# Optimization experiments

Measured on AMD Instinct MI355X. Metric: run time of the kernel, lower is better.

## Reference

```python
import jax, jax.numpy as jnp
import numpy as np

B, T, D, H = 2, 2048, 1024, 16
HD = D // H  # head_dim = 64


def setup_inputs() -> dict:
    key = jax.random.key(0)
    k1, k2, k3 = jax.random.split(key, 3)
    s = 0.02
    return {
        "x": jax.random.normal(k1, (B, T, D), dtype=jnp.float32),
        "Wqkv": jax.random.normal(k2, (D, 3 * D), dtype=jnp.float32) * s,
        "bqkv": jnp.zeros((3 * D,), dtype=jnp.float32),
        "Wout": jax.random.normal(k3, (D, D), dtype=jnp.float32) * s,
        "bout": jnp.zeros((D,), dtype=jnp.float32),
    }


def reference(x, Wqkv, bqkv, Wout, bout):
    Bx, Tx, Dx = x.shape
    qkv = x @ Wqkv + bqkv                                  # [B,T,3D]
    qkv = qkv.reshape(Bx, Tx, 3, H, HD)
    q, k, v = (jnp.moveaxis(qkv, 2, 0)[i] for i in range(3))  # each [B,T,H,HD]
    q = q.transpose(0, 2, 1, 3)  # [B,H,T,HD]
    k = k.transpose(0, 2, 1, 3)
    v = v.transpose(0, 2, 1, 3)
    scale = 1.0 / jnp.sqrt(jnp.float32(HD))
    attn = jnp.einsum("bhqd,bhkd->bhqk", q, k) * scale     # [B,H,T,T]
    causal = jnp.tril(jnp.ones((Tx, Tx), dtype=bool))
    attn = jnp.where(causal, attn, -jnp.inf)
    attn = jax.nn.softmax(attn, axis=-1)
    out = jnp.einsum("bhqk,bhkd->bhqd", attn, v)           # [B,H,T,HD]
    out = out.transpose(0, 2, 1, 3).reshape(Bx, Tx, Dx)
    return out @ Wout + bout
```

## Files before the change

### kernel.cpp

```cpp
#include <hip/hip_runtime.h>
#include <hip/hip_bf16.h>
#include <hip/hip_fp16.h>

typedef __attribute__((ext_vector_type(8))) short bf16x8;
typedef __attribute__((ext_vector_type(4))) float f32x4;
typedef unsigned short u16;
typedef unsigned int uint;

#define Bb 2
#define Tt 2048
#define Dd 1024
#define Hh 16

#define EXP2F(x) __builtin_amdgcn_exp2f(x)

__device__ inline u16 f2bf(float f) {
    union { float f; uint u; } v; v.f = f;
    uint r = v.u + 0x7fffu + ((v.u >> 16) & 1u);
    return (u16)(r >> 16);
}
__device__ inline uint fbits(float f) { union { float f; uint u; } v; v.f = f; return v.u; }
__device__ inline u16 f2h(float f) { return __half_as_ushort(__float2half(f)); }
__device__ inline float h2f(u16 u) { return __half2float(__ushort_as_half(u)); }

__device__ inline void glds16(const u16* g, u16* l) {
    __builtin_amdgcn_global_load_lds(
        (const __attribute__((address_space(1))) void*)g,
        (__attribute__((address_space(3))) void*)l,
        16, 0, 0);
}

__global__ __launch_bounds__(256) void cvt_bf16(
    const float* __restrict__ in, u16* __restrict__ out)
{
    const size_t i = ((size_t)blockIdx.x * 256 + threadIdx.x) * 8;
    const float4 a = *(const float4*)&in[i];
    const float4 b = *(const float4*)&in[i + 4];
    uint4 o;
    o.x = (uint)f2bf(a.x) | ((uint)f2bf(a.y) << 16);
    o.y = (uint)f2bf(a.z) | ((uint)f2bf(a.w) << 16);
    o.z = (uint)f2bf(b.x) | ((uint)f2bf(b.y) << 16);
    o.w = (uint)f2bf(b.z) | ((uint)f2bf(b.w) << 16);
    *(uint4*)&out[i] = o;
}

__global__ __launch_bounds__(256) void transpose_cvt(
    const float* __restrict__ W, u16* __restrict__ Wt, int K, int N)
{
    __shared__ float tile[64][65];
    const int k0 = blockIdx.y * 64, n0 = blockIdx.x * 64;
    const int tid = threadIdx.x;
    const int tr = tid >> 4;
    const int tc = (tid & 15) * 4;

    #pragma unroll
    for (int i = 0; i < 4; ++i) {
        const float4 v = *(const float4*)&W[(size_t)(k0 + tr + i * 16) * N + n0 + tc];
        tile[tr + i * 16][tc + 0] = v.x;
        tile[tr + i * 16][tc + 1] = v.y;
        tile[tr + i * 16][tc + 2] = v.z;
        tile[tr + i * 16][tc + 3] = v.w;
    }
    __syncthreads();
    #pragma unroll
    for (int i = 0; i < 4; ++i) {
        ushort4 o;
        o.x = f2bf(tile[tc + 0][tr + i * 16]);
        o.y = f2bf(tile[tc + 1][tr + i * 16]);
        o.z = f2bf(tile[tc + 2][tr + i * 16]);
        o.w = f2bf(tile[tc + 3][tr + i * 16]);
        *(ushort4*)&Wt[(size_t)(n0 + tr + i * 16) * K + k0 + tc] = o;
    }
}

template <int MODE>
__global__ __launch_bounds__(256) void gemm_bt(
    const u16* __restrict__ A, const u16* __restrict__ Bt,
    const float* __restrict__ bias, void* __restrict__ C,
    u16* __restrict__ vg, int M, int N, int K)
{
    __shared__ u16 As[2][128 * 32];
    __shared__ u16 Bs[2][128 * 32];

    const int tid  = threadIdx.x;
    const int lane = tid & 63;
    const int w    = tid >> 6;
    const int wm   = w >> 1, wn = w & 1;
    const int quad = lane >> 4;
    const int m16  = lane & 15;
    const int row0 = blockIdx.y * 128;
    const int col0 = blockIdx.x * 128;

    f32x4 acc[4][4];
    #pragma unroll
    for (int i = 0; i < 4; ++i)
        #pragma unroll
        for (int j = 0; j < 4; ++j) acc[i][j] = (f32x4){0.f, 0.f, 0.f, 0.f};

    const int sr  = tid >> 2, sqs = tid & 3;
    const int sq  = sqs ^ ((sr >> 1) & 3);
    const int ldsw = w * 512;
    const int slot = quad ^ ((m16 >> 1) & 3);

    const int nIter = K >> 5;

    glds16(&A [(size_t)(row0 + sr) * K + sq * 8],       &As[0][ldsw]);
    glds16(&A [(size_t)(row0 + sr + 64) * K + sq * 8],  &As[0][2048 + ldsw]);
    glds16(&Bt[(size_t)(col0 + sr) * K + sq * 8],       &Bs[0][ldsw]);
    glds16(&Bt[(size_t)(col0 + sr + 64) * K + sq * 8],  &Bs[0][2048 + ldsw]);

    for (int it = 0; it < nIter; ++it) {
        const int cb = it & 1;
        __syncthreads();

        if (it + 1 < nIter) {
            const int ko = (it + 1) << 5;
            const int nb = cb ^ 1;
            glds16(&A [(size_t)(row0 + sr) * K + ko + sq * 8],       &As[nb][ldsw]);
            glds16(&A [(size_t)(row0 + sr + 64) * K + ko + sq * 8],  &As[nb][2048 + ldsw]);
            glds16(&Bt[(size_t)(col0 + sr) * K + ko + sq * 8],       &Bs[nb][ldsw]);
            glds16(&Bt[(size_t)(col0 + sr + 64) * K + ko + sq * 8],  &Bs[nb][2048 + ldsw]);
        }

        bf16x8 af[4], bfr[4];
        #pragma unroll
        for (int mt = 0; mt < 4; ++mt)
            af[mt] = *(const bf16x8*)&As[cb][(wm * 64 + mt * 16 + m16) * 32 + slot * 8];
        #pragma unroll
        for (int nt = 0; nt < 4; ++nt)
            bfr[nt] = *(const bf16x8*)&Bs[cb][(wn * 64 + nt * 16 + m16) * 32 + slot * 8];
        #pragma unroll
        for (int mt = 0; mt < 4; ++mt)
            #pragma unroll
            for (int nt = 0; nt < 4; ++nt)
                acc[mt][nt] = __builtin_amdgcn_mfma_f32_16x16x32_bf16(
                    af[mt], bfr[nt], acc[mt][nt], 0, 0, 0);
    }

    #pragma unroll
    for (int mt = 0; mt < 4; ++mt) {
        #pragma unroll
        for (int nt = 0; nt < 4; ++nt) {
            const int row = row0 + wm * 64 + mt * 16 + quad * 4;
            const int col = col0 + wn * 64 + nt * 16 + m16;
            const float bv = bias[col];
            #pragma unroll
            for (int r = 0; r < 4; ++r) {
                const float v = acc[mt][nt][r] + bv;
                if (MODE == 0) {
                    ((float*)C)[(size_t)(row + r) * N + col] = v;
                } else {
                    if (col0 < 2048) {
                        ((u16*)C)[(size_t)(row + r) * 2048 + col] = f2bf(v);
                    } else {
                        const int hcol = col - 2048;
                        const int hh = hcol >> 6, dd = hcol & 63;
                        const int bb = (row + r) >> 11, tt = (row + r) & 2047;
                        vg[((size_t)(bb * Hh + hh) * 64 + dd) * Tt + tt] = f2bf(v);
                    }
                }
            }
        }
    }
}

__global__ __launch_bounds__(256, 4) void attn_split(
    const u16* __restrict__ qkvb, const u16* __restrict__ vglob,
    u16* __restrict__ wsO, float* __restrict__ wsL)
{
    const int hb  = blockIdx.x;
    const int h   = hb & 15, b = hb >> 4;
    const int qt  = 15 - (blockIdx.y >> 1);
    const int half = blockIdx.y & 1;
    const int tid = threadIdx.x;
    const int lane = tid & 63, w = tid >> 6;
    const int quad = lane >> 4, m16 = lane & 15;

    __shared__ u16 KV[2][64 * 64];
    __shared__ u16 Pt[128 * 72];

    const int q0 = qt * 128;
    const size_t qkbase = (size_t)(b * Tt) * 2048;
    const size_t vbase  = (size_t)((b * Hh + h) * 64) * Tt;

    const int sr8 = tid >> 3;
    const int sq8 = (tid & 7) ^ (sr8 & 7);
    const int ldsw = w * 512;
    const int slot = quad ^ (m16 & 7);

    bf16x8 qb[2][2];
    #pragma unroll
    for (int nt = 0; nt < 2; ++nt)
        #pragma unroll
        for (int ks = 0; ks < 2; ++ks)
            qb[nt][ks] = *(const bf16x8*)&qkvb[
                qkbase + (size_t)(q0 + w * 32 + nt * 16 + m16) * 2048
                + h * 64 + ks * 32 + quad * 8];

    f32x4 o[4][2];
    #pragma unroll
    for (int ct = 0; ct < 4; ++ct)
        #pragma unroll
        for (int nt = 0; nt < 2; ++nt) o[ct][nt] = (f32x4){0.f, 0.f, 0.f, 0.f};
    float ls[2] = {0.f, 0.f};
    const float sc2 = 0.125f * 1.4426950408889634f;

    const int ntiles = 2 * qt + 2;
    for (int kt = half; kt < ntiles; kt += 2) {
        const int k0 = kt * 64;
        __syncthreads();
        #pragma unroll
        for (int j = 0; j < 2; ++j) {
            const int row = j * 32 + sr8;
            glds16(&qkvb[qkbase + (size_t)(k0 + row) * 2048 + 1024 + h * 64 + sq8 * 8],
                   &KV[0][j * 2048 + ldsw]);
            glds16(&vglob[vbase + (size_t)row * Tt + k0 + sq8 * 8],
                   &KV[1][j * 2048 + ldsw]);
        }
        __syncthreads();

        if (k0 <= q0 + w * 32 + 31) {
            const u16* Ks = KV[0];
            const u16* Vt = KV[1];

            bf16x8 ak[4][2];
            #pragma unroll
            for (int mt = 0; mt < 4; ++mt) {
                const int ro = (mt * 16 + m16) * 64;
                ak[mt][0] = *(const bf16x8*)&Ks[ro + slot * 8];
                ak[mt][1] = *(const bf16x8*)&Ks[ro + (slot ^ 4) * 8];
            }
            f32x4 s[4][2];
            #pragma unroll
            for (int mt = 0; mt < 4; ++mt)
                #pragma unroll
                for (int nt = 0; nt < 2; ++nt) {
                    f32x4 a = (f32x4){0.f, 0.f, 0.f, 0.f};
                    a = __builtin_amdgcn_mfma_f32_16x16x32_bf16(ak[mt][0], qb[nt][0], a, 0, 0, 0);
                    a = __builtin_amdgcn_mfma_f32_16x16x32_bf16(ak[mt][1], qb[nt][1], a, 0, 0, 0);
                    s[mt][nt] = a;
                }

            const int qi0 = q0 + w * 32 + m16;
            const bool diag = (k0 + 63 > q0 + w * 32);
            #pragma unroll
            for (int mt = 0; mt < 4; ++mt)
                #pragma unroll
                for (int nt = 0; nt < 2; ++nt) {
                    float p[4];
                    const int kb = k0 + mt * 16 + quad * 4;
                    #pragma unroll
                    for (int r = 0; r < 4; ++r) {
                        float t = __builtin_fmaf(s[mt][nt][r], sc2, -8.0f);
                        if (diag) t = (kb + r <= qi0 + nt * 16) ? t : -1000.0f;
                        p[r] = EXP2F(t);
                    }
                    ls[nt] += (p[0] + p[1]) + (p[2] + p[3]);
                    uint2 pk;
                    pk.x = (fbits(p[0]) >> 16) | (fbits(p[1]) & 0xffff0000u);
                    pk.y = (fbits(p[2]) >> 16) | (fbits(p[3]) & 0xffff0000u);
                    *(uint2*)&Pt[(w * 32 + nt * 16 + m16) * 72 + mt * 16 + quad * 4] = pk;
                }

            bf16x8 av[4][2], pb[2][2];
            #pragma unroll
            for (int ct = 0; ct < 4; ++ct) {
                const int ro = (ct * 16 + m16) * 64;
                av[ct][0] = *(const bf16x8*)&Vt[ro + slot * 8];
                av[ct][1] = *(const bf16x8*)&Vt[ro + (slot ^ 4) * 8];
            }
            #pragma unroll
            for (int nt = 0; nt < 2; ++nt)
                #pragma unroll
                for (int ks = 0; ks < 2; ++ks)
                    pb[nt][ks] = *(const bf16x8*)&Pt[(w * 32 + nt * 16 + m16) * 72 + ks * 32 + quad * 8];
            #pragma unroll
            for (int ct = 0; ct < 4; ++ct)
                #pragma unroll
                for (int nt = 0; nt < 2; ++nt) {
                    o[ct][nt] = __builtin_amdgcn_mfma_f32_16x16x32_bf16(av[ct][0], pb[nt][0], o[ct][nt], 0, 0, 0);
                    o[ct][nt] = __builtin_amdgcn_mfma_f32_16x16x32_bf16(av[ct][1], pb[nt][1], o[ct][nt], 0, 0, 0);
                }
        }
    }

    #pragma unroll
    for (int nt = 0; nt < 2; ++nt) {
        ls[nt] += __shfl_xor(ls[nt], 16);
        ls[nt] += __shfl_xor(ls[nt], 32);
    }
    const int qrow = b * Tt + q0 + w * 32 + m16;
    if (quad == 0) {
        wsL[(half * Hh + h) * 4096 + qrow]      = ls[0];
        wsL[(half * Hh + h) * 4096 + qrow + 16] = ls[1];
    }
    #pragma unroll
    for (int ct = 0; ct < 4; ++ct)
        #pragma unroll
        for (int nt = 0; nt < 2; ++nt) {
            ushort4 pk;
            pk.x = f2h(o[ct][nt][0]);
            pk.y = f2h(o[ct][nt][1]);
            pk.z = f2h(o[ct][nt][2]);
            pk.w = f2h(o[ct][nt][3]);
            *(ushort4*)&wsO[((size_t)(half * 4096 + qrow + nt * 16)) * 1024
                            + h * 64 + ct * 16 + quad * 4] = pk;
        }
}

__global__ __launch_bounds__(256) void combine(
    const u16* __restrict__ wsO, const float* __restrict__ wsL,
    u16* __restrict__ attb)
{
    const int gi  = (blockIdx.x * 256 + threadIdx.x) * 8;
    const int row = gi >> 10;
    const int h   = (gi & 1023) >> 6;
    const float il = 1.0f / (wsL[h * 4096 + row] + wsL[(Hh + h) * 4096 + row]);
    const uint4 a = *(const uint4*)&wsO[gi];
    const uint4 c = *(const uint4*)&wsO[(size_t)4096 * 1024 + gi];
    const uint aw[4] = {a.x, a.y, a.z, a.w};
    const uint cw[4] = {c.x, c.y, c.z, c.w};
    uint ow[4];
    #pragma unroll
    for (int i = 0; i < 4; ++i) {
        const float r0 = (h2f((u16)(aw[i] & 0xffff)) + h2f((u16)(cw[i] & 0xffff))) * il;
        const float r1 = (h2f((u16)(aw[i] >> 16))    + h2f((u16)(cw[i] >> 16)))    * il;
        ow[i] = (uint)f2bf(r0) | ((uint)f2bf(r1) << 16);
    }
    uint4 o4; o4.x = ow[0]; o4.y = ow[1]; o4.z = ow[2]; o4.w = ow[3];
    *(uint4*)&attb[gi] = o4;
}

extern "C" void kernel_launch(void* const* d_in, const int* in_sizes, int n_in,
                              void* d_out, int out_size, void* d_ws, size_t ws_size,
                              hipStream_t stream) {
    const float* x    = (const float*)d_in[0];
    const float* Wqkv = (const float*)d_in[1];
    const float* bqkv = (const float*)d_in[2];
    const float* Wout = (const float*)d_in[3];
    const float* bout = (const float*)d_in[4];
    float* out = (float*)d_out;

    u16*   xb    = (u16*)d_ws;
    u16*   WqT   = xb    + (size_t)4096 * 1024;
    u16*   WoT   = WqT   + (size_t)3072 * 1024;
    u16*   qkvb  = WoT   + (size_t)1024 * 1024;
    u16*   attb  = qkvb  + (size_t)4096 * 2048;
    u16*   vglob = attb  + (size_t)4096 * 1024;
    u16*   wsO   = vglob + (size_t)4096 * 2048;
    float* wsL   = (float*)(wsO + (size_t)2 * 4096 * 1024);

    cvt_bf16<<<dim3((4096 * 1024) / 8 / 256), dim3(256), 0, stream>>>(x, xb);
    transpose_cvt<<<dim3(3072 / 64, 1024 / 64), dim3(256), 0, stream>>>(Wqkv, WqT, 1024, 3072);
    transpose_cvt<<<dim3(1024 / 64, 1024 / 64), dim3(256), 0, stream>>>(Wout, WoT, 1024, 1024);

    gemm_bt<1><<<dim3(3072 / 128, 4096 / 128), dim3(256), 0, stream>>>(
        xb, WqT, bqkv, qkvb, vglob, 4096, 3072, 1024);

    attn_split<<<dim3(Hh * Bb, 32), dim3(256), 0, stream>>>(qkvb, vglob, wsO, wsL);

    combine<<<dim3((4096 * 1024) / 8 / 256), dim3(256), 0, stream>>>(wsO, wsL, attb);

    gemm_bt<0><<<dim3(1024 / 128, 4096 / 128), dim3(256), 0, stream>>>(
        attb, WoT, bout, out, nullptr, 4096, 1024, 1024);
}
```

Baseline: 188.5 us.

## Triple-buffer GEMM LDS tiles with two-deep async prefetch and partial vmcnt waits

Moves the bf16 GEMM main loop from double to triple buffering in shared memory, issuing global-to-LDS loads two K-steps ahead. __syncthreads is replaced by an explicit s_waitcnt vmcnt(4) plus s_barrier, so only the oldest tile's loads must finish before compute. This hides more load latency behind MFMA work. In exchange LDS use grows by half, which can lower occupancy, and correctness depends on the hand-coded vmcnt count matching the number of outstanding loads.

```diff
diff --git a/kernel.cpp b/kernel.cpp
--- a/kernel.cpp
+++ b/kernel.cpp
@@ -79,8 +79,8 @@
     const float* __restrict__ bias, void* __restrict__ C,
     u16* __restrict__ vg, int M, int N, int K)
 {
-    __shared__ u16 As[2][128 * 32];
-    __shared__ u16 Bs[2][128 * 32];
+    __shared__ u16 As[3][128 * 32];
+    __shared__ u16 Bs[3][128 * 32];
 
     const int tid  = threadIdx.x;
     const int lane = tid & 63;
@@ -103,23 +103,34 @@
     const int slot = quad ^ ((m16 >> 1) & 3);
 
     const int nIter = K >> 5;
-
-    glds16(&A [(size_t)(row0 + sr) * K + sq * 8],       &As[0][ldsw]);
-    glds16(&A [(size_t)(row0 + sr + 64) * K + sq * 8],  &As[0][2048 + ldsw]);
-    glds16(&Bt[(size_t)(col0 + sr) * K + sq * 8],       &Bs[0][ldsw]);
-    glds16(&Bt[(size_t)(col0 + sr + 64) * K + sq * 8],  &Bs[0][2048 + ldsw]);
-
+    const u16* arow0 = &A [(size_t)(row0 + sr) * K + sq * 8];
+    const u16* arow1 = &A [(size_t)(row0 + sr + 64) * K + sq * 8];
+    const u16* brow0 = &Bt[(size_t)(col0 + sr) * K + sq * 8];
+    const u16* brow1 = &Bt[(size_t)(col0 + sr + 64) * K + sq * 8];
+
+    glds16(arow0,      &As[0][ldsw]);
+    glds16(arow1,      &As[0][2048 + ldsw]);
+    glds16(brow0,      &Bs[0][ldsw]);
+    glds16(brow1,      &Bs[0][2048 + ldsw]);
+    glds16(arow0 + 32, &As[1][ldsw]);
+    glds16(arow1 + 32, &As[1][2048 + ldsw]);
+    glds16(brow0 + 32, &Bs[1][ldsw]);
+    glds16(brow1 + 32, &Bs[1][2048 + ldsw]);
+
+    int cb = 0, pb = 2;
     for (int it = 0; it < nIter; ++it) {
-        const int cb = it & 1;
-        __syncthreads();
-
-        if (it + 1 < nIter) {
-            const int ko = (it + 1) << 5;
-            const int nb = cb ^ 1;
-            glds16(&A [(size_t)(row0 + sr) * K + ko + sq * 8],       &As[nb][ldsw]);
-            glds16(&A [(size_t)(row0 + sr + 64) * K + ko + sq * 8],  &As[nb][2048 + ldsw]);
-            glds16(&Bt[(size_t)(col0 + sr) * K + ko + sq * 8],       &Bs[nb][ldsw]);
-            glds16(&Bt[(size_t)(col0 + sr + 64) * K + ko + sq * 8],  &Bs[nb][2048 + ldsw]);
+        if (it + 1 < nIter)
+            asm volatile("s_waitcnt vmcnt(4)" ::: "memory");
+        else
+            asm volatile("s_waitcnt vmcnt(0)" ::: "memory");
+        asm volatile("s_barrier" ::: "memory");
+
+        if (it + 2 < nIter) {
+            const int ko = (it + 2) << 5;
+            glds16(arow0 + ko, &As[pb][ldsw]);
+            glds16(arow1 + ko, &As[pb][2048 + ldsw]);
+            glds16(brow0 + ko, &Bs[pb][ldsw]);
+            glds16(brow1 + ko, &Bs[pb][2048 + ldsw]);
         }
 
         bf16x8 af[4], bfr[4];
@@ -135,6 +146,9 @@
             for (int nt = 0; nt < 4; ++nt)
                 acc[mt][nt] = __builtin_amdgcn_mfma_f32_16x16x32_bf16(
                     af[mt], bfr[nt], acc[mt][nt], 0, 0, 0);
+
+        cb = (cb == 2) ? 0 : cb + 1;
+        pb = (pb == 2) ? 0 : pb + 1;
     }
 
     #pragma unroll
```

Result: no change. 190.0 us (+0.8%).
